# Kernel tuning notes

Measured on AMD Instinct MI355X. Metric: run time of the kernel, lower is better.

## Reference

```python
import jax, jax.numpy as jnp
import numpy as np


def setup_inputs() -> dict:
    key = jax.random.key(0)
    kq, kk, kv, kr, km = jax.random.split(key, 5)
    B, H, L, DK, DV = 4, 8, 2048, 32, 32
    Q = jax.random.normal(kq, (B, H, L, DK), dtype=jnp.float32)
    K = jax.random.normal(kk, (B, H, L, DK), dtype=jnp.float32)
    V = jax.random.normal(kv, (B, H, L, DV), dtype=jnp.float32)
    res_att = jax.random.normal(kr, (B, H, L, L), dtype=jnp.float32)
    attn_mask = jax.random.randint(km, (B, H, L, L), 0, 2).astype(bool)
    return {"Q": Q, "K": K, "V": V, "attn_mask": attn_mask, "res_att": res_att}


def reference(Q, K, V, attn_mask, res_att):
    d_k = Q.shape[-1]
    scale = 1.0 / np.sqrt(d_k).astype(np.float32)
    # scores: [B, H, Lq, Lk]
    scores = jnp.einsum("bhqd,bhkd->bhqk", Q, K) * scale + res_att
    scores = jnp.where(attn_mask, jnp.float32(-1e9), scores)
    attn = jax.nn.softmax(scores, axis=3)
    context = jnp.einsum("bhqk,bhkd->bhqd", attn, V)
    return (context, scores)
```

## Files before the change

kernel.cpp:

```cpp
#include <hip/hip_runtime.h>
#include <math.h>

#define LQ   2048
#define DKD  32
#define TQ   32
#define KT   128
#define NT   (LQ / KT)
#define KSTR 36
#define PSTR 132
#define CSTR 33

__global__ __launch_bounds__(256, 2)
void sdpa_fused(const float* __restrict__ Q,
                const float* __restrict__ K,
                const float* __restrict__ V,
                const int*   __restrict__ mask,
                const float* __restrict__ res,
                float* __restrict__ outCtx,
                float* __restrict__ outSc)
{
    __shared__ float Kt[KT * KSTR];
    __shared__ float Vt[KT * KSTR];
    __shared__ float Pt[TQ * PSTR];
    __shared__ float Qs[TQ * KSTR];
    __shared__ float mred[4 * TQ];
    __shared__ float lred[4 * TQ];

    const int t    = threadIdx.x;
    const int g    = t >> 6;
    const int lane = t & 63;
    const int qg   = lane >> 3;
    const int kg   = lane & 7;

    const int bx = blockIdx.x;
    const int bh = bx >> 6;
    const int qt = bx & 63;

    const long rowQ0 = (long)bh * LQ + (long)qt * TQ;

    {
        int q  = t >> 3;
        int d4 = (t & 7) << 2;
        float4 qv = *(const float4*)(Q + (rowQ0 + q) * DKD + d4);
        *(float4*)(Qs + q * KSTR + d4) = qv;
    }

    float m[4], l[4], acc[4][4];
    #pragma unroll
    for (int i = 0; i < 4; i++) {
        m[i] = -1e30f; l[i] = 0.f;
        acc[i][0] = acc[i][1] = acc[i][2] = acc[i][3] = 0.f;
    }

    const float scale = 0.17677669529663687f;

    for (int kt = 0; kt < NT; kt++) {
        __syncthreads();

        const long k0g = (long)bh * LQ + (long)kt * KT;
        float4 kst[4], vst[4];
        #pragma unroll
        for (int u = 0; u < 4; u++) {
            int f  = t + 256 * u;
            int kr = f >> 3;
            int d4 = (f & 7) << 2;
            kst[u] = *(const float4*)(K + (k0g + kr) * DKD + d4);
            vst[u] = *(const float4*)(V + (k0g + kr) * DKD + d4);
        }

        float rv[4][4]; int mv[4][4];
        const long colBase = (long)kt * KT + g * 32 + kg;
        #pragma unroll
        for (int i = 0; i < 4; i++) {
            const long rb = (rowQ0 + qg + 8*i) * (long)LQ + colBase;
            #pragma unroll
            for (int j = 0; j < 4; j++) {
                rv[i][j] = res[rb + 8*j];
                mv[i][j] = mask[rb + 8*j];
            }
        }

        #pragma unroll
        for (int u = 0; u < 4; u++) {
            int f  = t + 256 * u;
            int kr = f >> 3;
            int d4 = (f & 7) << 2;
            *(float4*)(Kt + kr * KSTR + d4) = kst[u];
            *(float4*)(Vt + kr * KSTR + d4) = vst[u];
        }
        __syncthreads();

        float S[4][4];
        #pragma unroll
        for (int i = 0; i < 4; i++) { S[i][0]=S[i][1]=S[i][2]=S[i][3]=0.f; }
        #pragma unroll
        for (int s = 0; s < 8; s++) {
            float4 qf[4], kf[4];
            #pragma unroll
            for (int i = 0; i < 4; i++)
                qf[i] = *(const float4*)(Qs + (qg + 8*i) * KSTR + 4*s);
            #pragma unroll
            for (int j = 0; j < 4; j++)
                kf[j] = *(const float4*)(Kt + (g*32 + kg + 8*j) * KSTR + 4*s);
            #pragma unroll
            for (int i = 0; i < 4; i++) {
                #pragma unroll
                for (int j = 0; j < 4; j++) {
                    S[i][j] += qf[i].x * kf[j].x;
                    S[i][j] += qf[i].y * kf[j].y;
                    S[i][j] += qf[i].z * kf[j].z;
                    S[i][j] += qf[i].w * kf[j].w;
                }
            }
        }

        #pragma unroll
        for (int i = 0; i < 4; i++) {
            const long rb = (rowQ0 + qg + 8*i) * (long)LQ + colBase;
            #pragma unroll
            for (int j = 0; j < 4; j++) {
                float sv = S[i][j] * scale + rv[i][j];
                sv = mv[i][j] ? -1e9f : sv;
                S[i][j] = sv;
                outSc[rb + 8*j] = sv;
            }
        }

        #pragma unroll
        for (int i = 0; i < 4; i++) {
            float mloc = fmaxf(fmaxf(S[i][0], S[i][1]), fmaxf(S[i][2], S[i][3]));
            mloc = fmaxf(mloc, __shfl_xor(mloc, 1));
            mloc = fmaxf(mloc, __shfl_xor(mloc, 2));
            mloc = fmaxf(mloc, __shfl_xor(mloc, 4));
            float mn = fmaxf(m[i], mloc);
            float al = __expf(m[i] - mn);
            m[i] = mn;
            float ps = 0.f;
            #pragma unroll
            for (int j = 0; j < 4; j++) {
                float p = __expf(S[i][j] - mn);
                Pt[(qg + 8*i) * PSTR + g*32 + kg + 8*j] = p;
                ps += p;
            }
            ps += __shfl_xor(ps, 1);
            ps += __shfl_xor(ps, 2);
            ps += __shfl_xor(ps, 4);
            l[i] = l[i] * al + ps;
            acc[i][0] *= al; acc[i][1] *= al; acc[i][2] *= al; acc[i][3] *= al;
        }

        #pragma unroll
        for (int s2 = 0; s2 < 8; s2++) {
            const int kk = g*32 + 4*s2;
            float4 pf[4];
            #pragma unroll
            for (int i = 0; i < 4; i++)
                pf[i] = *(const float4*)(Pt + (qg + 8*i) * PSTR + kk);
            #pragma unroll
            for (int j2 = 0; j2 < 4; j2++) {
                float4 vf = *(const float4*)(Vt + (kk + j2) * KSTR + 4*kg);
                #pragma unroll
                for (int i = 0; i < 4; i++) {
                    float p = (j2 == 0) ? pf[i].x : (j2 == 1) ? pf[i].y
                            : (j2 == 2) ? pf[i].z : pf[i].w;
                    acc[i][0] += p * vf.x;
                    acc[i][1] += p * vf.y;
                    acc[i][2] += p * vf.z;
                    acc[i][3] += p * vf.w;
                }
            }
        }
    }

    __syncthreads();
    #pragma unroll
    for (int i = 0; i < 4; i++) {
        float* c = Pt + g * (TQ * CSTR) + (qg + 8*i) * CSTR + 4*kg;
        c[0] = acc[i][0]; c[1] = acc[i][1]; c[2] = acc[i][2]; c[3] = acc[i][3];
        if (kg == 0) {
            mred[g * TQ + qg + 8*i] = m[i];
            lred[g * TQ + qg + 8*i] = l[i];
        }
    }
    __syncthreads();
    {
        int q  = t >> 3;
        int d4 = (t & 7) << 2;
        float m0 = mred[q], m1 = mred[TQ + q], m2 = mred[2*TQ + q], m3 = mred[3*TQ + q];
        float mm = fmaxf(fmaxf(m0, m1), fmaxf(m2, m3));
        float w0 = __expf(m0 - mm), w1 = __expf(m1 - mm);
        float w2 = __expf(m2 - mm), w3 = __expf(m3 - mm);
        float lt = lred[q]*w0 + lred[TQ+q]*w1 + lred[2*TQ+q]*w2 + lred[3*TQ+q]*w3;
        float inv = 1.0f / lt;
        const float* c0 = Pt + 0*(TQ*CSTR) + q*CSTR + d4;
        const float* c1 = Pt + 1*(TQ*CSTR) + q*CSTR + d4;
        const float* c2 = Pt + 2*(TQ*CSTR) + q*CSTR + d4;
        const float* c3 = Pt + 3*(TQ*CSTR) + q*CSTR + d4;
        float4 o;
        o.x = (c0[0]*w0 + c1[0]*w1 + c2[0]*w2 + c3[0]*w3) * inv;
        o.y = (c0[1]*w0 + c1[1]*w1 + c2[1]*w2 + c3[1]*w3) * inv;
        o.z = (c0[2]*w0 + c1[2]*w1 + c2[2]*w2 + c3[2]*w3) * inv;
        o.w = (c0[3]*w0 + c1[3]*w1 + c2[3]*w2 + c3[3]*w3) * inv;
        *(float4*)(outCtx + (rowQ0 + q) * DKD + d4) = o;
    }
}

extern "C" void kernel_launch(void* const* d_in, const int* in_sizes, int n_in,
                              void* d_out, int out_size, void* d_ws, size_t ws_size,
                              hipStream_t stream) {
    const float* Q    = (const float*)d_in[0];
    const float* K    = (const float*)d_in[1];
    const float* V    = (const float*)d_in[2];
    const int*   mask = (const int*)d_in[3];
    const float* res  = (const float*)d_in[4];
    float* outCtx = (float*)d_out;
    float* outSc  = (float*)d_out + (size_t)4 * 8 * 2048 * 32;
    sdpa_fused<<<dim3(2048), dim3(256), 0, stream>>>(Q, K, V, mask, res, outCtx, outSc);
}
```

Before: 1.644 ms.

## Use direct global-to-LDS loads, XOR-swizzled LDS, vectorized score/mask I/O

K and V tiles now go straight into shared memory with global_load_lds instead of passing through registers. LDS layouts are XOR-swizzled instead of padded, and the P buffer is aliased onto the K tile, which shrinks LDS so occupancy can rise to four blocks per CU. Column ownership changes so each thread reads res and mask and writes scores as contiguous float4 values instead of strided scalars. Blocks are also remapped across XCDs and indexing is narrowed to 32-bit. The risks are correctness of the swizzle and aliasing under the new syncs, and register pressure under the tighter launch bound.

```diff
diff --git a/kernel.cpp b/kernel.cpp
--- a/kernel.cpp
+++ b/kernel.cpp
@@ -6,11 +6,16 @@
 #define TQ   32
 #define KT   128
 #define NT   (LQ / KT)
-#define KSTR 36
-#define PSTR 132
-#define CSTR 33
-
-__global__ __launch_bounds__(256, 2)
+
+
+__device__ __forceinline__ void gload_lds16(const float* g, float* l) {
+    __builtin_amdgcn_global_load_lds(
+        (__attribute__((address_space(1))) void*)g,
+        (__attribute__((address_space(3))) void*)l,
+        16, 0, 0);
+}
+
+__global__ __launch_bounds__(256, 4)
 void sdpa_fused(const float* __restrict__ Q,
                 const float* __restrict__ K,
                 const float* __restrict__ V,
@@ -19,10 +24,9 @@
                 float* __restrict__ outCtx,
                 float* __restrict__ outSc)
 {
-    __shared__ float Kt[KT * KSTR];
-    __shared__ float Vt[KT * KSTR];
-    __shared__ float Pt[TQ * PSTR];
-    __shared__ float Qs[TQ * KSTR];
+    __shared__ __align__(16) float Qs[TQ * 32];
+    __shared__ __align__(16) float KP[KT * 32];
+    __shared__ __align__(16) float Vt[KT * 32];
     __shared__ float mred[4 * TQ];
     __shared__ float lred[4 * TQ];
 
@@ -32,17 +36,17 @@
     const int qg   = lane >> 3;
     const int kg   = lane & 7;
 
-    const int bx = blockIdx.x;
+    const int bx = (blockIdx.x & 7) * 256 + (blockIdx.x >> 3);
     const int bh = bx >> 6;
     const int qt = bx & 63;
 
-    const long rowQ0 = (long)bh * LQ + (long)qt * TQ;
+    const int rowQ0 = bh * LQ + qt * TQ;
 
     {
         int q  = t >> 3;
-        int d4 = (t & 7) << 2;
-        float4 qv = *(const float4*)(Q + (rowQ0 + q) * DKD + d4);
-        *(float4*)(Qs + q * KSTR + d4) = qv;
+        int db = t & 7;
+        float4 qv = *(const float4*)(Q + (rowQ0 + q) * DKD + (db << 2));
+        *(float4*)(Qs + q * 32 + (((db ^ q) & 7) << 2)) = qv;
     }
 
     float m[4], l[4], acc[4][4];
@@ -53,42 +57,44 @@
     }
 
     const float scale = 0.17677669529663687f;
+    const int wb = (t >> 6) << 6;
 
     for (int kt = 0; kt < NT; kt++) {
         __syncthreads();
 
-        const long k0g = (long)bh * LQ + (long)kt * KT;
-        float4 kst[4], vst[4];
+        const int k0g = bh * LQ + kt * KT;
         #pragma unroll
         for (int u = 0; u < 4; u++) {
-            int f  = t + 256 * u;
-            int kr = f >> 3;
-            int d4 = (f & 7) << 2;
-            kst[u] = *(const float4*)(K + (k0g + kr) * DKD + d4);
-            vst[u] = *(const float4*)(V + (k0g + kr) * DKD + d4);
-        }
-
-        float rv[4][4]; int mv[4][4];
-        const long colBase = (long)kt * KT + g * 32 + kg;
-        #pragma unroll
-        for (int i = 0; i < 4; i++) {
-            const long rb = (rowQ0 + qg + 8*i) * (long)LQ + colBase;
-            #pragma unroll
-            for (int j = 0; j < 4; j++) {
-                rv[i][j] = res[rb + 8*j];
-                mv[i][j] = mask[rb + 8*j];
-            }
-        }
-
-        #pragma unroll
-        for (int u = 0; u < 4; u++) {
-            int f  = t + 256 * u;
-            int kr = f >> 3;
-            int d4 = (f & 7) << 2;
-            *(float4*)(Kt + kr * KSTR + d4) = kst[u];
-            *(float4*)(Vt + kr * KSTR + d4) = vst[u];
-        }
+            int f   = t + 256 * u;
+            int kr  = f >> 3;
+            int dbs = (f ^ (kr >> 2)) & 7;
+            const float* gk = K + (k0g + kr) * DKD + (dbs << 2);
+            const float* gv = V + (k0g + kr) * DKD + (dbs << 2);
+            float* lbase = (float*)0;
+            int fb = (wb + 256 * u) << 2;
+            lbase = KP + fb;  gload_lds16(gk, lbase);
+            lbase = Vt + fb;  gload_lds16(gv, lbase);
+        }
+
+        const int colBase = kt * KT + g * 32 + (kg << 2);
+        float4 rv4[4]; int4 mv4[4];
+        #pragma unroll
+        for (int i = 0; i < 4; i++) {
+            const int rb = (rowQ0 + qg + 8*i) * LQ + colBase;
+            rv4[i] = *(const float4*)(res + rb);
+            mv4[i] = *(const int4*)(mask + rb);
+        }
+
         __syncthreads();
+
+        int mbits = 0;
+        #pragma unroll
+        for (int i = 0; i < 4; i++) {
+            mbits |= (mv4[i].x != 0) << (4*i);
+            mbits |= (mv4[i].y != 0) << (4*i + 1);
+            mbits |= (mv4[i].z != 0) << (4*i + 2);
+            mbits |= (mv4[i].w != 0) << (4*i + 3);
+        }
 
         float S[4][4];
         #pragma unroll
@@ -98,10 +104,12 @@
             float4 qf[4], kf[4];
             #pragma unroll
             for (int i = 0; i < 4; i++)
-                qf[i] = *(const float4*)(Qs + (qg + 8*i) * KSTR + 4*s);
-            #pragma unroll
-            for (int j = 0; j < 4; j++)
-                kf[j] = *(const float4*)(Kt + (g*32 + kg + 8*j) * KSTR + 4*s);
+                qf[i] = *(const float4*)(Qs + (qg + 8*i) * 32 + (((s ^ qg) & 7) << 2));
+            #pragma unroll
+            for (int j = 0; j < 4; j++) {
+                int r = g * 32 + (kg << 2) + j;
+                kf[j] = *(const float4*)(KP + r * 32 + (((s ^ kg) & 7) << 2));
+            }
             #pragma unroll
             for (int i = 0; i < 4; i++) {
                 #pragma unroll
@@ -116,14 +124,15 @@
 
         #pragma unroll
         for (int i = 0; i < 4; i++) {
-            const long rb = (rowQ0 + qg + 8*i) * (long)LQ + colBase;
-            #pragma unroll
-            for (int j = 0; j < 4; j++) {
-                float sv = S[i][j] * scale + rv[i][j];
-                sv = mv[i][j] ? -1e9f : sv;
-                S[i][j] = sv;
-                outSc[rb + 8*j] = sv;
-            }
+            const int rb  = (rowQ0 + qg + 8*i) * LQ + colBase;
+            const int msk = mbits >> (4*i);
+            float4 sv;
+            sv.x = (msk & 1)        ? -1e9f : (S[i][0] * scale + rv4[i].x);
+            sv.y = ((msk >> 1) & 1) ? -1e9f : (S[i][1] * scale + rv4[i].y);
+            sv.z = ((msk >> 2) & 1) ? -1e9f : (S[i][2] * scale + rv4[i].z);
+            sv.w = ((msk >> 3) & 1) ? -1e9f : (S[i][3] * scale + rv4[i].w);
+            *(float4*)(outSc + rb) = sv;
+            S[i][0] = sv.x; S[i][1] = sv.y; S[i][2] = sv.z; S[i][3] = sv.w;
         }
 
         #pragma unroll
@@ -135,13 +144,14 @@
             float mn = fmaxf(m[i], mloc);
             float al = __expf(m[i] - mn);
             m[i] = mn;
-            float ps = 0.f;
-            #pragma unroll
-            for (int j = 0; j < 4; j++) {
-                float p = __expf(S[i][j] - mn);
-                Pt[(qg + 8*i) * PSTR + g*32 + kg + 8*j] = p;
-                ps += p;
-            }
+            float4 p;
+            p.x = __expf(S[i][0] - mn);
+            p.y = __expf(S[i][1] - mn);
+            p.z = __expf(S[i][2] - mn);
+            p.w = __expf(S[i][3] - mn);
+            int row = qg + 8*i;
+            *(float4*)(KP + (g << 10) + row * 32 + (((kg ^ qg) & 7) << 2)) = p;
+            float ps = p.x + p.y + p.z + p.w;
             ps += __shfl_xor(ps, 1);
             ps += __shfl_xor(ps, 2);
             ps += __shfl_xor(ps, 4);
@@ -151,14 +161,15 @@
 
         #pragma unroll
         for (int s2 = 0; s2 < 8; s2++) {
-            const int kk = g*32 + 4*s2;
             float4 pf[4];
             #pragma unroll
             for (int i = 0; i < 4; i++)
-                pf[i] = *(const float4*)(Pt + (qg + 8*i) * PSTR + kk);
+                pf[i] = *(const float4*)(KP + (g << 10) + (qg + 8*i) * 32
+                                            + (((s2 ^ qg) & 7) << 2));
             #pragma unroll
             for (int j2 = 0; j2 < 4; j2++) {
-                float4 vf = *(const float4*)(Vt + (kk + j2) * KSTR + 4*kg);
+                int r = g * 32 + (s2 << 2) + j2;
+                float4 vf = *(const float4*)(Vt + r * 32 + (((kg ^ s2) & 7) << 2));
                 #pragma unroll
                 for (int i = 0; i < 4; i++) {
                     float p = (j2 == 0) ? pf[i].x : (j2 == 1) ? pf[i].y
@@ -172,36 +183,37 @@
         }
     }
 
-    __syncthreads();
     #pragma unroll
     for (int i = 0; i < 4; i++) {
-        float* c = Pt + g * (TQ * CSTR) + (qg + 8*i) * CSTR + 4*kg;
-        c[0] = acc[i][0]; c[1] = acc[i][1]; c[2] = acc[i][2]; c[3] = acc[i][3];
+        int row = qg + 8*i;
+        float4 cv; cv.x = acc[i][0]; cv.y = acc[i][1]; cv.z = acc[i][2]; cv.w = acc[i][3];
+        *(float4*)(KP + (g << 10) + row * 32 + (((kg ^ qg) & 7) << 2)) = cv;
         if (kg == 0) {
-            mred[g * TQ + qg + 8*i] = m[i];
-            lred[g * TQ + qg + 8*i] = l[i];
+            mred[g * TQ + row] = m[i];
+            lred[g * TQ + row] = l[i];
         }
     }
     __syncthreads();
     {
         int q  = t >> 3;
-        int d4 = (t & 7) << 2;
+        int db = t & 7;
         float m0 = mred[q], m1 = mred[TQ + q], m2 = mred[2*TQ + q], m3 = mred[3*TQ + q];
         float mm = fmaxf(fmaxf(m0, m1), fmaxf(m2, m3));
         float w0 = __expf(m0 - mm), w1 = __expf(m1 - mm);
         float w2 = __expf(m2 - mm), w3 = __expf(m3 - mm);
         float lt = lred[q]*w0 + lred[TQ+q]*w1 + lred[2*TQ+q]*w2 + lred[3*TQ+q]*w3;
         float inv = 1.0f / lt;
-        const float* c0 = Pt + 0*(TQ*CSTR) + q*CSTR + d4;
-        const float* c1 = Pt + 1*(TQ*CSTR) + q*CSTR + d4;
-        const float* c2 = Pt + 2*(TQ*CSTR) + q*CSTR + d4;
-        const float* c3 = Pt + 3*(TQ*CSTR) + q*CSTR + d4;
+        int co = q * 32 + (((db ^ q) & 7) << 2);
+        float4 c0 = *(const float4*)(KP + co);
+        float4 c1 = *(const float4*)(KP + 1024 + co);
+        float4 c2 = *(const float4*)(KP + 2048 + co);
+        float4 c3 = *(const float4*)(KP + 3072 + co);
         float4 o;
-        o.x = (c0[0]*w0 + c1[0]*w1 + c2[0]*w2 + c3[0]*w3) * inv;
-        o.y = (c0[1]*w0 + c1[1]*w1 + c2[1]*w2 + c3[1]*w3) * inv;
-        o.z = (c0[2]*w0 + c1[2]*w1 + c2[2]*w2 + c3[2]*w3) * inv;
-        o.w = (c0[3]*w0 + c1[3]*w1 + c2[3]*w2 + c3[3]*w3) * inv;
-        *(float4*)(outCtx + (rowQ0 + q) * DKD + d4) = o;
+        o.x = (c0.x*w0 + c1.x*w1 + c2.x*w2 + c3.x*w3) * inv;
+        o.y = (c0.y*w0 + c1.y*w1 + c2.y*w2 + c3.y*w3) * inv;
+        o.z = (c0.z*w0 + c1.z*w1 + c2.z*w2 + c3.z*w3) * inv;
+        o.w = (c0.w*w0 + c1.w*w1 + c2.w*w2 + c3.w*w3) * inv;
+        *(float4*)(outCtx + (rowQ0 + q) * DKD + (db << 2)) = o;
     }
 }
 
```

Result: slower. 4.493 ms (+173.2%).
